# Kernel optimization log

Hardware: AMD Instinct MI355X
Metric: run time of the kernel (lower is better)

Reference implementation:

```python
import jax, jax.numpy as jnp
import numpy as np

B, A, N, L = 4, 16, 8, 512
DE, DH, H, C = 256, 64, 8, 1.0
DHEAD = DE // H
LN_EPS = 1e-5

def _layernorm(x, w, b):
    mu = jnp.mean(x, axis=-1, keepdims=True)
    var = jnp.mean((x - mu) ** 2, axis=-1, keepdims=True)
    return (x - mu) / jnp.sqrt(var + LN_EPS) * w + b

def _logmap0(x, c):
    sc = jnp.sqrt(c)
    n = jnp.maximum(jnp.linalg.norm(x, axis=-1, keepdims=True), 1e-15)
    u = jnp.minimum(sc * n, 1.0 - 1e-5)  # stay inside artanh domain
    return jnp.arctanh(u) * x / (sc * n)

def _expmap0(u, c):
    sc = jnp.sqrt(c)
    n = jnp.maximum(jnp.linalg.norm(u, axis=-1, keepdims=True), 1e-15)
    return jnp.tanh(sc * n) * u / (sc * n)

def setup_inputs() -> dict:
    key = jax.random.key(0)
    ks = jax.random.split(key, 5)
    curr_rho = jax.random.normal(ks[0], (B, A, DE), jnp.float32)
    demo_rho = jax.random.normal(ks[1], (B, N, L, A, DE), jnp.float32)
    demo_hyp = jax.random.normal(ks[2], (B, N, L, DH), jnp.float32)
    # project hyperbolic points inside the unit Poincare ball
    demo_hyp = demo_hyp / (1.0 + jnp.linalg.norm(demo_hyp, axis=-1, keepdims=True)) * 0.9
    demo_mask = jnp.ones((B, N, L), jnp.int32)
    Wq = jax.random.normal(ks[3], (DE, DE), jnp.float32) / np.sqrt(DE)
    Wk = jax.random.normal(ks[4], (DE, DE), jnp.float32) / np.sqrt(DE)
    return {"curr_rho": curr_rho, "demo_rho": demo_rho, "demo_hyp": demo_hyp,
            "demo_mask": demo_mask, "Wq": Wq, "Wk": Wk,
            "ln_q_w": jnp.ones((DE,), jnp.float32), "ln_q_b": jnp.zeros((DE,), jnp.float32),
            "ln_k_w": jnp.ones((DE,), jnp.float32), "ln_k_b": jnp.zeros((DE,), jnp.float32)}

def reference(curr_rho, demo_rho, demo_hyp, demo_mask, Wq, Wk, ln_q_w, ln_q_b, ln_k_w, ln_k_b):
    # queries: [B,H,A,dh]
    q = (_layernorm(curr_rho, ln_q_w, ln_q_b) @ Wq.T).reshape(B, A, H, DHEAD).transpose(0, 2, 1, 3)
    # keys: [B,N,L,A,H,dh]; the original gather over agents with arange(A) is identity,
    # so scores align query agent a with key agent a directly.
    k = (_layernorm(demo_rho, ln_k_w, ln_k_b) @ Wk.T).reshape(B, N, L, A, H, DHEAD)
    scores = jnp.einsum('bhad,bnlahd->bhanl', q, k) / np.sqrt(DHEAD)  # [B,H,A,N,L]
    dm = demo_mask[:, None, None, :, :]
    scores = jnp.where(dm == 0, -jnp.inf, scores)
    attn_flat = jax.nn.softmax(scores.reshape(B, H, A, N * L), axis=-1)
    # Poincare weighted mean in tangent space at origin
    vals_tan0 = _logmap0(demo_hyp.reshape(B, N * L, DH), C)          # [B,NL,dh_h]
    m_h = jnp.einsum('bhax,bxd->bhad', attn_flat, vals_tan0)          # [B,H,A,d_h]
    y_h_tan0 = _logmap0(_expmap0(m_h, C), C)
    curr_hyp = _expmap0(jnp.mean(y_h_tan0, axis=1), C)                # [B,A,d_h]
    max_rad = 1.0 / np.sqrt(C) - 1e-5
    norm = jnp.maximum(jnp.linalg.norm(curr_hyp, axis=-1, keepdims=True), 1e-6)
    curr_hyp = curr_hyp * jnp.minimum(max_rad / norm, 1.0)
    curr_hyp = jnp.mean(curr_hyp, axis=1)                             # [B,d_h] (as in source)
    return curr_hyp, attn_flat.reshape(B, H, A, N, L)
```

## Files before the change

### kernel.cpp

```cpp
#include <hip/hip_runtime.h>
#include <math.h>

#define LN_EPS_ 1e-5f
#define INV_SQRT_DHEAD 0.17677669529663687f


__device__ __forceinline__ float waveReduceSum(float v) {
    #pragma unroll
    for (int m = 32; m > 0; m >>= 1) v += __shfl_xor(v, m, 64);
    return v;
}
__device__ __forceinline__ float waveReduceMax(float v) {
    #pragma unroll
    for (int m = 32; m > 0; m >>= 1) v = fmaxf(v, __shfl_xor(v, m, 64));
    return v;
}

__global__ __launch_bounds__(256) void k_prep(
    const float* __restrict__ curr_rho, const float* __restrict__ Wq,
    const float* __restrict__ Wk, const float* __restrict__ lnqw,
    const float* __restrict__ lnqb, const float* __restrict__ lnkw,
    const float* __restrict__ lnkb,
    float* __restrict__ g, float* __restrict__ s0, float* __restrict__ s2)
{
    __shared__ float xs[256];
    __shared__ float qs[256];
    __shared__ float red[8];
    const int t = threadIdx.x;
    const int w = t >> 6;
    const int ba = blockIdx.x;
    const float x = curr_rho[(size_t)ba * 256 + t];

    float sm = waveReduceSum(x);
    if ((t & 63) == 0) red[w] = sm;
    __syncthreads();
    const float mu = (red[0] + red[1] + red[2] + red[3]) * (1.0f / 256.0f);
    __syncthreads();
    const float dx = x - mu;
    float sq = waveReduceSum(dx * dx);
    if ((t & 63) == 0) red[w] = sq;
    __syncthreads();
    const float var = (red[0] + red[1] + red[2] + red[3]) * (1.0f / 256.0f);
    const float rstd = 1.0f / sqrtf(var + LN_EPS_);
    __syncthreads();
    xs[t] = dx * rstd * lnqw[t] + lnqb[t];
    __syncthreads();

    {
        const float4* wq4 = (const float4*)(Wq + (size_t)t * 256);
        float acc = 0.f;
        #pragma unroll 8
        for (int e4 = 0; e4 < 64; ++e4) {
            float4 wv = wq4[e4];
            acc += xs[e4*4+0]*wv.x + xs[e4*4+1]*wv.y + xs[e4*4+2]*wv.z + xs[e4*4+3]*wv.w;
        }
        qs[t] = acc;
    }
    __syncthreads();

    for (int h = 0; h < 8; ++h) {
        float qk = 0.f;
        #pragma unroll 8
        for (int dh = 0; dh < 32; ++dh)
            qk += qs[h*32+dh] * Wk[(size_t)(h*32+dh)*256 + t];
        const float gv = lnkw[t] * qk;
        const float b2 = lnkb[t] * qk;
        g[((size_t)ba * 8 + h) * 256 + t] = gv;
        float sg = waveReduceSum(gv);
        float sb = waveReduceSum(b2);
        if ((t & 63) == 0) { red[w] = sg; red[4 + w] = sb; }
        __syncthreads();
        if (t == 0) {
            s0[ba*8+h] = red[0] + red[1] + red[2] + red[3];
            s2[ba*8+h] = red[4] + red[5] + red[6] + red[7];
        }
        __syncthreads();
    }
}

__global__ __launch_bounds__(256) void k_vals(
    const float* __restrict__ demo_hyp, float* __restrict__ vals)
{
    const int t = threadIdx.x;
    const size_t idx = (size_t)blockIdx.x * 256 + t;
    const float x = demo_hyp[idx];
    const float ss = waveReduceSum(x * x);
    const float nrm = sqrtf(ss);
    const float n = fmaxf(nrm, 1e-15f);
    const float u = fminf(n, 1.0f - 1e-5f);
    const float f = atanhf(u) / n;
    vals[idx] = x * f;
}

__global__ __launch_bounds__(256) void k_scores(
    const float* __restrict__ demo_rho, const int* __restrict__ demo_mask,
    const float* __restrict__ g, const float* __restrict__ s0,
    const float* __restrict__ s2, float* __restrict__ attn)
{
    __shared__ float sbuf[8][132];
    const int t = threadIdx.x;
    const int gid = blockIdx.x;
    const int lc = gid & 3;
    const int n  = (gid >> 2) & 7;
    const int a  = (gid >> 5) & 15;
    const int b  = gid >> 9;
    const int c  = t & 31;
    const int r  = t >> 5;

    float gr[8][8];
    {
        const float* gb = g + ((size_t)(b*16 + a) * 8) * 256 + c * 8;
        #pragma unroll
        for (int h = 0; h < 8; ++h) {
            float4 ga = *(const float4*)(gb + h * 256);
            float4 gc = *(const float4*)(gb + h * 256 + 4);
            gr[h][0]=ga.x; gr[h][1]=ga.y; gr[h][2]=ga.z; gr[h][3]=ga.w;
            gr[h][4]=gc.x; gr[h][5]=gc.y; gr[h][6]=gc.z; gr[h][7]=gc.w;
        }
    }
    const float s0v = s0[(b*16 + a) * 8 + (c & 7)];
    const float s2v = s2[(b*16 + a) * 8 + (c & 7)];
    const int* mrow = demo_mask + (b*8 + n) * 512 + lc * 128;

    const float* xbase = demo_rho +
        ((size_t)((b*8 + n) * 512 + lc * 128) * 16 + a) * 256 + c * 8;

    #pragma unroll 2
    for (int p = 0; p < 16; ++p) {
        const float* xp = xbase + (size_t)(p * 8 + r) * 4096;
        float4 xa = *(const float4*)(xp);
        float4 xb = *(const float4*)(xp + 4);
        float xv[8] = {xa.x, xa.y, xa.z, xa.w, xb.x, xb.y, xb.z, xb.w};

        float v[10];
        #pragma unroll
        for (int h = 0; h < 8; ++h) {
            float acc = 0.f;
            #pragma unroll
            for (int j = 0; j < 8; ++j) acc += xv[j] * gr[h][j];
            v[h] = acc;
        }
        float sm = 0.f, sq = 0.f;
        #pragma unroll
        for (int j = 0; j < 8; ++j) { sm += xv[j]; sq += xv[j] * xv[j]; }
        v[8] = sm; v[9] = sq;

        #pragma unroll
        for (int m = 1; m <= 16; m <<= 1) {
            #pragma unroll
            for (int i = 0; i < 10; ++i) v[i] += __shfl_xor(v[i], m, 32);
        }

        if (c < 8) {
            const float mu   = v[8] * (1.0f / 256.0f);
            const float var  = v[9] * (1.0f / 256.0f) - mu * mu;
            const float rstd = 1.0f / sqrtf(var + LN_EPS_);
            float sc = (rstd * (v[c] - mu * s0v) + s2v) * INV_SQRT_DHEAD;
            const int lidx = p * 8 + r;
            if (mrow[lidx] == 0) sc = -INFINITY;
            sbuf[c][lidx] = sc;
        }
    }
    __syncthreads();
    {
        const int h = t >> 5;
        const float* rowp = &sbuf[h][0];
        float4 vout = *(const float4*)(rowp + c * 4);
        const size_t off = (size_t)((b*8 + h) * 16 + a) * 4096 + n * 512 + lc * 128 + c * 4;
        *(float4*)(attn + off) = vout;
    }
}

__global__ __launch_bounds__(256) void k_softmax_mh(
    float* __restrict__ attn, const float* __restrict__ vals,
    float* __restrict__ mh)
{
    __shared__ float p0[4096];
    __shared__ float p1[4096];
    __shared__ float red[4];
    __shared__ float mpart[4][64];
    const int t = threadIdx.x;
    const int w = t >> 6;
    const int row0 = blockIdx.x * 2;
    const int b = row0 >> 7;

    for (int rr = 0; rr < 2; ++rr) {
        const int row = row0 + rr;
        float* dst = attn + (size_t)row * 4096;
        float* pl = rr ? p1 : p0;
        float lmax = -INFINITY;
        float4 v4[4];
        #pragma unroll
        for (int k = 0; k < 4; ++k) {
            float4 vv = ((const float4*)dst)[k * 256 + t];
            v4[k] = vv;
            lmax = fmaxf(lmax, fmaxf(fmaxf(vv.x, vv.y), fmaxf(vv.z, vv.w)));
        }
        lmax = waveReduceMax(lmax);
        if ((t & 63) == 0) red[w] = lmax;
        __syncthreads();
        const float mx = fmaxf(fmaxf(red[0], red[1]), fmaxf(red[2], red[3]));
        __syncthreads();
        float lsum = 0.f;
        #pragma unroll
        for (int k = 0; k < 4; ++k) {
            float4 vv = v4[k];
            vv.x = __expf(vv.x - mx); vv.y = __expf(vv.y - mx);
            vv.z = __expf(vv.z - mx); vv.w = __expf(vv.w - mx);
            v4[k] = vv;
            lsum += vv.x + vv.y + vv.z + vv.w;
        }
        lsum = waveReduceSum(lsum);
        if ((t & 63) == 0) red[w] = lsum;
        __syncthreads();
        const float inv = 1.0f / (red[0] + red[1] + red[2] + red[3]);
        __syncthreads();
        #pragma unroll
        for (int k = 0; k < 4; ++k) {
            float4 vv = v4[k];
            vv.x *= inv; vv.y *= inv; vv.z *= inv; vv.w *= inv;
            ((float4*)pl)[k * 256 + t] = vv;
            ((float4*)dst)[k * 256 + t] = vv;
        }
    }
    __syncthreads();

    const int ch = t >> 6, d = t & 63;
    const float* vb = vals + (size_t)b * 4096 * 64 + d;
    float acc0a = 0.f, acc0b = 0.f, acc1a = 0.f, acc1b = 0.f;
    const int x0 = ch * 1024;
    #pragma unroll 16
    for (int x = x0; x < x0 + 1024; x += 2) {
        const float va = vb[(size_t)x * 64];
        const float vc = vb[(size_t)(x + 1) * 64];
        acc0a += p0[x] * va;     acc0b += p0[x + 1] * vc;
        acc1a += p1[x] * va;     acc1b += p1[x + 1] * vc;
    }
    const float acc0 = acc0a + acc0b;
    const float acc1 = acc1a + acc1b;
    for (int rr = 0; rr < 2; ++rr) {
        mpart[ch][d] = rr ? acc1 : acc0;
        __syncthreads();
        if (t < 64) {
            const float m = mpart[0][t] + mpart[1][t] + mpart[2][t] + mpart[3][t];
            mh[(size_t)(row0 + rr) * 64 + t] = m;
        }
        __syncthreads();
    }
}

__global__ __launch_bounds__(1024) void k_final(
    const float* __restrict__ mh, float* __restrict__ out)
{
    __shared__ float contrib[16][64];
    const int t = threadIdx.x;
    const int a = t >> 6, d = t & 63;
    const int b = blockIdx.x;
    float accY = 0.f;
    #pragma unroll
    for (int h = 0; h < 8; ++h) {
        const float m = mh[(size_t)((b*8 + h) * 16 + a) * 64 + d];
        const float ss = waveReduceSum(m * m);
        const float nm = sqrtf(ss);
        const float n1 = fmaxf(nm, 1e-15f);
        const float t1 = tanhf(n1);
        const float e  = t1 * m / n1;
        const float ne = t1 * nm / n1;
        const float n2 = fmaxf(ne, 1e-15f);
        const float u  = fminf(n2, 1.0f - 1e-5f);
        accY += atanhf(u) * e / n2;
    }
    const float ym = accY * 0.125f;
    const float ssy = waveReduceSum(ym * ym);
    const float nmy = sqrtf(ssy);
    const float n3 = fmaxf(nmy, 1e-15f);
    const float t3 = tanhf(n3);
    const float chv = t3 * ym / n3;
    const float nch = t3 * nmy / n3;
    const float nrm = fmaxf(nch, 1e-6f);
    const float sc = fminf((1.0f - 1e-5f) / nrm, 1.0f);
    contrib[a][d] = chv * sc;
    __syncthreads();
    if (t < 64) {
        float s = 0.f;
        #pragma unroll
        for (int a2 = 0; a2 < 16; ++a2) s += contrib[a2][t];
        out[b * 64 + t] = s * (1.0f / 16.0f);
    }
}

extern "C" void kernel_launch(void* const* d_in, const int* in_sizes, int n_in,
                              void* d_out, int out_size, void* d_ws, size_t ws_size,
                              hipStream_t stream) {
    const float* curr_rho  = (const float*)d_in[0];
    const float* demo_rho  = (const float*)d_in[1];
    const float* demo_hyp  = (const float*)d_in[2];
    const int*   demo_mask = (const int*)d_in[3];
    const float* Wq   = (const float*)d_in[4];
    const float* Wk   = (const float*)d_in[5];
    const float* lnqw = (const float*)d_in[6];
    const float* lnqb = (const float*)d_in[7];
    const float* lnkw = (const float*)d_in[8];
    const float* lnkb = (const float*)d_in[9];

    float* out  = (float*)d_out;
    float* attn = out + 256;

    float* ws   = (float*)d_ws;
    float* g    = ws;
    float* s0   = ws + 131072;
    float* s2   = ws + 131584;
    float* vals = ws + 132096;
    float* mh   = ws + 1180672;

    hipLaunchKernelGGL(k_prep, dim3(64), dim3(256), 0, stream,
                       curr_rho, Wq, Wk, lnqw, lnqb, lnkw, lnkb, g, s0, s2);
    hipLaunchKernelGGL(k_vals, dim3(4096), dim3(256), 0, stream, demo_hyp, vals);
    hipLaunchKernelGGL(k_scores, dim3(2048), dim3(256), 0, stream,
                       demo_rho, demo_mask, g, s0, s2, attn);
    hipLaunchKernelGGL(k_softmax_mh, dim3(256), dim3(256), 0, stream, attn, vals, mh);
    hipLaunchKernelGGL(k_final, dim3(4), dim3(1024), 0, stream, mh, out);
}
```

Before: 458.7 us.

## Restructure score reduction with 16-lane groups, prefetch, and vectorized attention-value product

The scores kernel now assigns 16 lanes per key row, so each row is reduced with fewer shuffles using a split-and-select reduction that packs eight head sums plus the two LayerNorm moments into five values. It also software-prefetches the next row's inputs and requests two blocks per CU. The softmax/value kernel reads vals as float4 per thread and reduces across lanes with shuffles instead of scalar strided loads. The aim is to cut shuffle count and improve load vectorization on the memory-bound demo_rho stream, at the cost of more registers and more complex lane/head selection logic.

```diff
diff --git a/kernel.cpp b/kernel.cpp
--- a/kernel.cpp
+++ b/kernel.cpp
@@ -92,7 +92,7 @@
     vals[idx] = x * f;
 }
 
-__global__ __launch_bounds__(256) void k_scores(
+__global__ __launch_bounds__(256, 2) void k_scores(
     const float* __restrict__ demo_rho, const int* __restrict__ demo_mask,
     const float* __restrict__ g, const float* __restrict__ s0,
     const float* __restrict__ s2, float* __restrict__ attn)
@@ -104,69 +104,106 @@
     const int n  = (gid >> 2) & 7;
     const int a  = (gid >> 5) & 15;
     const int b  = gid >> 9;
-    const int c  = t & 31;
-    const int r  = t >> 5;
-
-    float gr[8][8];
+    const int lane = t & 63;
+    const int wv   = t >> 6;
+    const int c    = lane & 15;
+    const int rowg = lane >> 4;
+
+    float4 gr[8][4];
     {
-        const float* gb = g + ((size_t)(b*16 + a) * 8) * 256 + c * 8;
-        #pragma unroll
-        for (int h = 0; h < 8; ++h) {
-            float4 ga = *(const float4*)(gb + h * 256);
-            float4 gc = *(const float4*)(gb + h * 256 + 4);
-            gr[h][0]=ga.x; gr[h][1]=ga.y; gr[h][2]=ga.z; gr[h][3]=ga.w;
-            gr[h][4]=gc.x; gr[h][5]=gc.y; gr[h][6]=gc.z; gr[h][7]=gc.w;
-        }
-    }
-    const float s0v = s0[(b*16 + a) * 8 + (c & 7)];
-    const float s2v = s2[(b*16 + a) * 8 + (c & 7)];
+        const float* gb = g + ((size_t)(b*16 + a) * 8) * 256 + c * 4;
+        #pragma unroll
+        for (int h = 0; h < 8; ++h)
+            #pragma unroll
+            for (int k = 0; k < 4; ++k)
+                gr[h][k] = *(const float4*)(gb + h * 256 + k * 64);
+    }
+    const bool active = (c < 5) || (c >= 8 && c < 11);
+    const int  h_eff  = (c < 8) ? ((c < 5) ? c : 0) : ((c < 11) ? c - 3 : 0);
+    const float s0v = s0[(b*16 + a) * 8 + h_eff];
+    const float s2v = s2[(b*16 + a) * 8 + h_eff];
     const int* mrow = demo_mask + (b*8 + n) * 512 + lc * 128;
 
     const float* xbase = demo_rho +
-        ((size_t)((b*8 + n) * 512 + lc * 128) * 16 + a) * 256 + c * 8;
-
-    #pragma unroll 2
-    for (int p = 0; p < 16; ++p) {
-        const float* xp = xbase + (size_t)(p * 8 + r) * 4096;
-        float4 xa = *(const float4*)(xp);
-        float4 xb = *(const float4*)(xp + 4);
-        float xv[8] = {xa.x, xa.y, xa.z, xa.w, xb.x, xb.y, xb.z, xb.w};
+        ((size_t)((b*8 + n) * 512 + lc * 128) * 16 + a) * 256 + c * 4;
+
+    float4 xk[4];
+    {
+        const float* xp = xbase + (size_t)(wv * 4 + rowg) * 4096;
+        #pragma unroll
+        for (int k = 0; k < 4; ++k) xk[k] = *(const float4*)(xp + k * 64);
+    }
+
+    for (int p = 0; p < 8; ++p) {
+        const int row = p * 16 + wv * 4 + rowg;
+        float4 xn[4];
+        if (p < 7) {
+            const float* xp = xbase + (size_t)(row + 16) * 4096;
+            #pragma unroll
+            for (int k = 0; k < 4; ++k) xn[k] = *(const float4*)(xp + k * 64);
+        }
 
         float v[10];
         #pragma unroll
         for (int h = 0; h < 8; ++h) {
             float acc = 0.f;
             #pragma unroll
-            for (int j = 0; j < 8; ++j) acc += xv[j] * gr[h][j];
+            for (int k = 0; k < 4; ++k) {
+                acc += xk[k].x * gr[h][k].x + xk[k].y * gr[h][k].y
+                     + xk[k].z * gr[h][k].z + xk[k].w * gr[h][k].w;
+            }
             v[h] = acc;
         }
-        float sm = 0.f, sq = 0.f;
-        #pragma unroll
-        for (int j = 0; j < 8; ++j) { sm += xv[j]; sq += xv[j] * xv[j]; }
-        v[8] = sm; v[9] = sq;
-
-        #pragma unroll
-        for (int m = 1; m <= 16; m <<= 1) {
-            #pragma unroll
-            for (int i = 0; i < 10; ++i) v[i] += __shfl_xor(v[i], m, 32);
-        }
-
-        if (c < 8) {
-            const float mu   = v[8] * (1.0f / 256.0f);
-            const float var  = v[9] * (1.0f / 256.0f) - mu * mu;
+        {
+            float sm = 0.f, sq = 0.f;
+            #pragma unroll
+            for (int k = 0; k < 4; ++k) {
+                sm += xk[k].x + xk[k].y + xk[k].z + xk[k].w;
+                sq += xk[k].x*xk[k].x + xk[k].y*xk[k].y
+                    + xk[k].z*xk[k].z + xk[k].w*xk[k].w;
+            }
+            v[8] = sm; v[9] = sq;
+        }
+
+        #pragma unroll
+        for (int i = 0; i < 10; ++i) v[i] += __shfl_xor(v[i], 8, 16);
+        const bool hi = (c & 8);
+        float w5[5];
+        #pragma unroll
+        for (int j = 0; j < 5; ++j) w5[j] = hi ? v[5 + j] : v[j];
+        #pragma unroll
+        for (int m = 4; m > 0; m >>= 1)
+            #pragma unroll
+            for (int j = 0; j < 5; ++j) w5[j] += __shfl_xor(w5[j], m, 16);
+        const float t3 = __shfl_xor(w5[3], 8, 16);
+        const float t4 = __shfl_xor(w5[4], 8, 16);
+        const float sumv = hi ? w5[3] : t3;
+        const float sqv  = hi ? w5[4] : t4;
+
+        if (active) {
+            float sel = w5[0];
+            sel = ((c & 7) == 1) ? w5[1] : sel;
+            sel = ((c & 7) == 2) ? w5[2] : sel;
+            sel = (c == 3) ? w5[3] : sel;
+            sel = (c == 4) ? w5[4] : sel;
+            const float mu   = sumv * (1.0f / 256.0f);
+            const float var  = sqv * (1.0f / 256.0f) - mu * mu;
             const float rstd = 1.0f / sqrtf(var + LN_EPS_);
-            float sc = (rstd * (v[c] - mu * s0v) + s2v) * INV_SQRT_DHEAD;
-            const int lidx = p * 8 + r;
-            if (mrow[lidx] == 0) sc = -INFINITY;
-            sbuf[c][lidx] = sc;
-        }
+            float sc = (rstd * (sel - mu * s0v) + s2v) * INV_SQRT_DHEAD;
+            if (mrow[row] == 0) sc = -INFINITY;
+            sbuf[h_eff][row] = sc;
+        }
+
+        #pragma unroll
+        for (int k = 0; k < 4; ++k) xk[k] = xn[k];
     }
     __syncthreads();
     {
         const int h = t >> 5;
+        const int c32 = t & 31;
         const float* rowp = &sbuf[h][0];
-        float4 vout = *(const float4*)(rowp + c * 4);
-        const size_t off = (size_t)((b*8 + h) * 16 + a) * 4096 + n * 512 + lc * 128 + c * 4;
+        float4 vout = *(const float4*)(rowp + c32 * 4);
+        const size_t off = (size_t)((b*8 + h) * 16 + a) * 4096 + n * 512 + lc * 128 + c32 * 4;
         *(float4*)(attn + off) = vout;
     }
 }
@@ -178,7 +215,7 @@
     __shared__ float p0[4096];
     __shared__ float p1[4096];
     __shared__ float red[4];
-    __shared__ float mpart[4][64];
+    __shared__ float wpart[4 * 2 * 64];
     const int t = threadIdx.x;
     const int w = t >> 6;
     const int row0 = blockIdx.x * 2;
@@ -225,27 +262,36 @@
     }
     __syncthreads();
 
-    const int ch = t >> 6, d = t & 63;
-    const float* vb = vals + (size_t)b * 4096 * 64 + d;
-    float acc0a = 0.f, acc0b = 0.f, acc1a = 0.f, acc1b = 0.f;
-    const int x0 = ch * 1024;
-    #pragma unroll 16
-    for (int x = x0; x < x0 + 1024; x += 2) {
-        const float va = vb[(size_t)x * 64];
-        const float vc = vb[(size_t)(x + 1) * 64];
-        acc0a += p0[x] * va;     acc0b += p0[x + 1] * vc;
-        acc1a += p1[x] * va;     acc1b += p1[x + 1] * vc;
-    }
-    const float acc0 = acc0a + acc0b;
-    const float acc1 = acc1a + acc1b;
-    for (int rr = 0; rr < 2; ++rr) {
-        mpart[ch][d] = rr ? acc1 : acc0;
-        __syncthreads();
-        if (t < 64) {
-            const float m = mpart[0][t] + mpart[1][t] + mpart[2][t] + mpart[3][t];
-            mh[(size_t)(row0 + rr) * 64 + t] = m;
-        }
-        __syncthreads();
+    const int ch = t >> 4, d4 = t & 15;
+    const float* vb = vals + (size_t)b * 4096 * 64 + d4 * 4;
+    float4 a0 = {0,0,0,0}, a1 = {0,0,0,0};
+    const int x0 = ch * 256;
+    #pragma unroll 4
+    for (int x = x0; x < x0 + 256; ++x) {
+        const float4 vv = *(const float4*)(vb + (size_t)x * 64);
+        const float q0 = p0[x], q1 = p1[x];
+        a0.x += q0 * vv.x; a0.y += q0 * vv.y; a0.z += q0 * vv.z; a0.w += q0 * vv.w;
+        a1.x += q1 * vv.x; a1.y += q1 * vv.y; a1.z += q1 * vv.z; a1.w += q1 * vv.w;
+    }
+    #pragma unroll
+    for (int m = 16; m <= 32; m <<= 1) {
+        a0.x += __shfl_xor(a0.x, m, 64); a0.y += __shfl_xor(a0.y, m, 64);
+        a0.z += __shfl_xor(a0.z, m, 64); a0.w += __shfl_xor(a0.w, m, 64);
+        a1.x += __shfl_xor(a1.x, m, 64); a1.y += __shfl_xor(a1.y, m, 64);
+        a1.z += __shfl_xor(a1.z, m, 64); a1.w += __shfl_xor(a1.w, m, 64);
+    }
+    if ((t & 63) < 16) {
+        float* wp0 = wpart + (w * 2 + 0) * 64 + d4 * 4;
+        float* wp1 = wpart + (w * 2 + 1) * 64 + d4 * 4;
+        wp0[0] = a0.x; wp0[1] = a0.y; wp0[2] = a0.z; wp0[3] = a0.w;
+        wp1[0] = a1.x; wp1[1] = a1.y; wp1[2] = a1.z; wp1[3] = a1.w;
+    }
+    __syncthreads();
+    if (t < 128) {
+        const int rr = t >> 6, d = t & 63;
+        const float m = wpart[(0 * 2 + rr) * 64 + d] + wpart[(1 * 2 + rr) * 64 + d]
+                      + wpart[(2 * 2 + rr) * 64 + d] + wpart[(3 * 2 + rr) * 64 + d];
+        mh[(size_t)(row0 + rr) * 64 + d] = m;
     }
 }
 
```

Result: no change. 461.2 us (+0.5%).
